# Kernel tuning notes

Measured on AMD Instinct MI355X. Metric: run time of the kernel, lower is better.

Reference implementation:

```python
import jax, jax.numpy as jnp
import numpy as np

N_PATHOLOGY = 14      # NUM_PATHOLOGY_NODES (CheXpert/NIH pathology count)
NEG_SLOPE = 0.2       # PyG GATv2Conv default negative_slope


def gatv2_layer(x, src, dst, n_nodes, Wl, bl, Wr, br, att, bias, concat):
    """PyG GATv2Conv (share_weights=False, dropout inactive in eval).
    Wl/bl: source (lin_l) transform; Wr/br: target (lin_r) transform.
    att: [H, C] attention vector; bias: output bias.
    """
    H, C = att.shape
    xl = (x @ Wl + bl).reshape(-1, H, C)   # [N, H, C] source features
    xr = (x @ Wr + br).reshape(-1, H, C)   # [N, H, C] target features
    xj = xl[src]                            # [E, H, C] gathered source msgs
    xi = xr[dst]                            # [E, H, C] gathered targets
    s = jax.nn.leaky_relu(xi + xj, NEG_SLOPE)
    e = jnp.einsum('ehc,hc->eh', s, att)    # [E, H] raw attention logits
    # segment softmax over incoming edges of each destination node
    m = jax.ops.segment_max(e, dst, num_segments=n_nodes)      # [N, H]
    e = jnp.exp(e - m[dst])
    denom = jax.ops.segment_sum(e, dst, num_segments=n_nodes)  # [N, H]
    alpha = e / (denom[dst] + 1e-16)
    out = jax.ops.segment_sum(alpha[:, :, None] * xj, dst, num_segments=n_nodes)
    out = out.reshape(n_nodes, H * C) if concat else out.mean(axis=1)
    return out + bias


def setup_inputs() -> dict:
    key = jax.random.key(0)
    ks = jax.random.split(key, 16)
    N, E, D, H = 10000, 50000, 768, 4
    s = 0.02
    inp = {
        'x': jax.random.normal(ks[0], (N, D), jnp.float32),
        'edge_index': jax.random.randint(ks[1], (2, E), 0, N, jnp.int32),
        # layer 1: in=768 -> heads=4, out=768 (concat -> 3072)
        'Wl1': jax.random.normal(ks[2], (D, H * D), jnp.float32) * s,
        'bl1': jnp.zeros((H * D,), jnp.float32),
        'Wr1': jax.random.normal(ks[3], (D, H * D), jnp.float32) * s,
        'br1': jnp.zeros((H * D,), jnp.float32),
        'att1': jax.random.normal(ks[4], (H, D), jnp.float32) * s,
        'bias1': jnp.zeros((H * D,), jnp.float32),
        # layer 2: in=3072 -> heads=1, out=768 (mean/no-concat)
        'Wl2': jax.random.normal(ks[5], (H * D, D), jnp.float32) * s,
        'bl2': jnp.zeros((D,), jnp.float32),
        'Wr2': jax.random.normal(ks[6], (H * D, D), jnp.float32) * s,
        'br2': jnp.zeros((D,), jnp.float32),
        'att2': jax.random.normal(ks[7], (1, D), jnp.float32) * s,
        'bias2': jnp.zeros((D,), jnp.float32),
    }
    return inp


def reference(x, edge_index, Wl1, bl1, Wr1, br1, att1, bias1,
              Wl2, bl2, Wr2, br2, att2, bias2):
    n = x.shape[0]
    # PyG GATv2Conv adds self loops by default
    loops = jnp.arange(n, dtype=edge_index.dtype)
    src = jnp.concatenate([edge_index[0], loops])
    dst = jnp.concatenate([edge_index[1], loops])
    h = gatv2_layer(x, src, dst, n, Wl1, bl1, Wr1, br1, att1, bias1, True)
    h = jax.nn.relu(h)  # dropout is identity in eval mode
    out = gatv2_layer(h, src, dst, n, Wl2, bl2, Wr2, br2, att2, bias2, False)
    return out[:N_PATHOLOGY]
```

## Files before the change

kernel.cpp:

```cpp
#include <hip/hip_runtime.h>
#include <cstdint>
#include <cstddef>

#define N_PATH 14
#define NEG_SLOPE 0.2f
#define BINW 128
#define NZ2 4

using u16 = unsigned short;
using u32 = unsigned int;
typedef __attribute__((ext_vector_type(4))) float f32x4;
typedef __attribute__((ext_vector_type(8))) short bf16x8;

__device__ __forceinline__ float lrelu(float v) { return v > 0.f ? v : NEG_SLOPE * v; }
__device__ __forceinline__ u16 f2bf(float f) {
    union { float f; u32 u; } c; c.f = f;
    return (u16)((c.u + 0x7FFFu + ((c.u >> 16) & 1u)) >> 16);
}
__device__ __forceinline__ float bf2f(u16 v) {
    union { u32 u; float f; } c; c.u = ((u32)v) << 16; return c.f;
}
__device__ __forceinline__ int imin(int a, int b) { return a < b ? a : b; }

__global__ void k_init(int* __restrict__ mapBC, int nMap,
                       u32* __restrict__ z, int nZ)
{
    int stride = gridDim.x * blockDim.x;
    int i0 = blockIdx.x * blockDim.x + threadIdx.x;
    for (int i = i0; i < nMap; i += stride) mapBC[i] = -1;
    for (int i = i0; i < nZ; i += stride) z[i] = 0;
}

__global__ void k_build2(const int* __restrict__ esrc, const int* __restrict__ edst,
                         int E, int Nn,
                         int* __restrict__ mapB, int* __restrict__ listB,
                         int* __restrict__ cnt,
                         int* __restrict__ deg2, int* __restrict__ e2bin,
                         int capB)
{
    int e = blockIdx.x * blockDim.x + threadIdx.x;
    int ET = E + Nn;
    if (e >= ET) return;
    int s, d;
    if (e < E) { s = esrc[e]; d = edst[e]; } else { s = e - E; d = s; }
    if (d >= N_PATH) return;
    int slot = atomicAdd(&deg2[d], 1);
    if (slot < BINW) e2bin[d * BINW + slot] = s;
    int old = atomicCAS(&mapB[s], -1, -2);
    if (old == -1) {
        int idx = atomicAdd(&cnt[0], 1);
        if (idx < capB) listB[idx] = s;
        mapB[s] = idx;
    }
}

__global__ void k_build1(const int* __restrict__ esrc, const int* __restrict__ edst,
                         int E, int Nn, const float* __restrict__ x,
                         const int* __restrict__ mapB,
                         int* __restrict__ mapC,
                         int* __restrict__ cnt,
                         int* __restrict__ deg1, int* __restrict__ e1bin,
                         u16* __restrict__ Abf,
                         int capB, int capC)
{
    int e = blockIdx.x * blockDim.x + threadIdx.x;
    int ET = E + Nn;
    int lane = threadIdx.x & 63;

    int s = 0;
    int idx = -1;
    if (e < ET) {
        int d;
        if (e < E) { s = esrc[e]; d = edst[e]; } else { s = e - E; d = s; }
        int b = mapB[d];
        if (b >= 0 && b < capB) {
            int slot = atomicAdd(&deg1[b], 1);
            if (slot < BINW) e1bin[b * BINW + slot] = s;
            int old = atomicCAS(&mapC[s], -1, -2);
            if (old == -1) {
                idx = atomicAdd(&cnt[1], 1);
                mapC[s] = idx;
            }
        }
    }

    bool win = (idx >= 0 && idx < capC);
    unsigned long long mask = __ballot(win);
    while (mask) {
        int l = (int)(__ffsll((long long)mask) - 1);
        mask &= mask - 1;
        int wnode = __shfl(s, l);
        int wslot = __shfl(idx, l);
        const float* xr = x + (size_t)wnode * 768 + lane * 12;
        u16* dst = Abf + (size_t)wslot * 768 + lane * 12;
        float4 v0 = *reinterpret_cast<const float4*>(xr);
        float4 v1 = *reinterpret_cast<const float4*>(xr + 4);
        float4 v2 = *reinterpret_cast<const float4*>(xr + 8);
        uint2 o0, o1, o2;
        o0.x = (u32)f2bf(v0.x) | ((u32)f2bf(v0.y) << 16);
        o0.y = (u32)f2bf(v0.z) | ((u32)f2bf(v0.w) << 16);
        o1.x = (u32)f2bf(v1.x) | ((u32)f2bf(v1.y) << 16);
        o1.y = (u32)f2bf(v1.z) | ((u32)f2bf(v1.w) << 16);
        o2.x = (u32)f2bf(v2.x) | ((u32)f2bf(v2.y) << 16);
        o2.y = (u32)f2bf(v2.z) | ((u32)f2bf(v2.w) << 16);
        *reinterpret_cast<uint2*>(dst)     = o0;
        *reinterpret_cast<uint2*>(dst + 4) = o1;
        *reinterpret_cast<uint2*>(dst + 8) = o2;
    }
}

__device__ __forceinline__
void stage_W(const float* __restrict__ W, int ldw, int wKoff, int n0,
             u16* __restrict__ Ws, int nthreads)
{
    int t = threadIdx.x;
    for (int idx = t; idx < 768 * 8; idx += nthreads) {
        int n4 = (idx & 7) << 2;
        int k  = idx >> 3;
        float4 wv = *reinterpret_cast<const float4*>(
            W + (size_t)(wKoff + k) * ldw + n0 + n4);
        int c = (k >> 3) & 7, kl = k & 7;
        int chbase = (k >> 6) * 2048;
        float wa[4] = {wv.x, wv.y, wv.z, wv.w};
        #pragma unroll
        for (int i = 0; i < 4; ++i) {
            int n = n4 + i;
            Ws[chbase + n * 64 + (kl | ((c ^ (n & 7)) << 3))] = f2bf(wa[i]);
        }
    }
}

__global__ __launch_bounds__(512)
void k_gemm1(const u16* __restrict__ Abf,
             const int* __restrict__ listB, const int* __restrict__ mapC,
             const float* __restrict__ Wl1, const float* __restrict__ Wr1,
             const float* __restrict__ bl1, const float* __restrict__ br1,
             u16* __restrict__ XL1, u16* __restrict__ XR1,
             const int* __restrict__ cnt, int capC, int capB)
{
    __shared__ __align__(16) u16 Ws[12 * 2048];
    int blk = blockIdx.x;
    bool isR = blk >= 96;
    int n0 = (isR ? blk - 96 : blk) * 32;
    const float* W    = isR ? Wr1 : Wl1;
    const float* bias = isR ? br1 : bl1;
    u16* Cout = isR ? XR1 : XL1;
    int nC = imin(cnt[1], capC);
    int M  = isR ? imin(cnt[0], capB) : nC;

    stage_W(W, 3072, 0, n0, Ws, 512);
    __syncthreads();

    int t = threadIdx.x;
    int wave = t >> 6, lane = t & 63;
    int lrow = lane & 15, lhi = lane >> 4;
    int x0 = lrow & 7;
    int preB0 = lrow * 64;
    int preB1 = (16 + lrow) * 64;

    float bv0 = bias[n0 + lrow];
    float bv1 = bias[n0 + 16 + lrow];

    int ntiles = (M + 63) >> 6;
    for (int rt = wave; rt < ntiles; rt += 8) {
        const u16* ap0; const u16* ap1; const u16* ap2; const u16* ap3;
        {
            int ar0 = rt * 64 + lrow;       if (ar0 >= M) ar0 = M - 1;
            int ar1 = ar0 + 16;             if (ar1 >= M) ar1 = M - 1;
            int ar2 = rt * 64 + 32 + lrow;  if (ar2 >= M) ar2 = M - 1;
            int ar3 = ar2 + 16;             if (ar3 >= M) ar3 = M - 1;
            int g0 = ar0, g1 = ar1, g2 = ar2, g3 = ar3;
            if (isR) {
                g0 = mapC[listB[ar0]]; if (g0 < 0) g0 = 0; if (g0 >= nC) g0 = nC - 1;
                g1 = mapC[listB[ar1]]; if (g1 < 0) g1 = 0; if (g1 >= nC) g1 = nC - 1;
                g2 = mapC[listB[ar2]]; if (g2 < 0) g2 = 0; if (g2 >= nC) g2 = nC - 1;
                g3 = mapC[listB[ar3]]; if (g3 < 0) g3 = 0; if (g3 >= nC) g3 = nC - 1;
            }
            ap0 = Abf + (size_t)g0 * 768 + lhi * 8;
            ap1 = Abf + (size_t)g1 * 768 + lhi * 8;
            ap2 = Abf + (size_t)g2 * 768 + lhi * 8;
            ap3 = Abf + (size_t)g3 * 768 + lhi * 8;
        }

        f32x4 acc00 = {0,0,0,0}, acc01 = {0,0,0,0};
        f32x4 acc10 = {0,0,0,0}, acc11 = {0,0,0,0};
        f32x4 acc20 = {0,0,0,0}, acc21 = {0,0,0,0};
        f32x4 acc30 = {0,0,0,0}, acc31 = {0,0,0,0};

        #pragma unroll 4
        for (int kst = 0; kst < 24; ++kst) {
            int ch = kst >> 1;
            int sw = ((((kst & 1) << 2) | lhi) ^ x0) << 3;
            bf16x8 b0 = *reinterpret_cast<const bf16x8*>(&Ws[ch * 2048 + preB0 + sw]);
            bf16x8 b1 = *reinterpret_cast<const bf16x8*>(&Ws[ch * 2048 + preB1 + sw]);
            bf16x8 a0 = *reinterpret_cast<const bf16x8*>(ap0 + kst * 32);
            bf16x8 a1 = *reinterpret_cast<const bf16x8*>(ap1 + kst * 32);
            bf16x8 a2 = *reinterpret_cast<const bf16x8*>(ap2 + kst * 32);
            bf16x8 a3 = *reinterpret_cast<const bf16x8*>(ap3 + kst * 32);
            acc00 = __builtin_amdgcn_mfma_f32_16x16x32_bf16(a0, b0, acc00, 0, 0, 0);
            acc01 = __builtin_amdgcn_mfma_f32_16x16x32_bf16(a0, b1, acc01, 0, 0, 0);
            acc10 = __builtin_amdgcn_mfma_f32_16x16x32_bf16(a1, b0, acc10, 0, 0, 0);
            acc11 = __builtin_amdgcn_mfma_f32_16x16x32_bf16(a1, b1, acc11, 0, 0, 0);
            acc20 = __builtin_amdgcn_mfma_f32_16x16x32_bf16(a2, b0, acc20, 0, 0, 0);
            acc21 = __builtin_amdgcn_mfma_f32_16x16x32_bf16(a2, b1, acc21, 0, 0, 0);
            acc30 = __builtin_amdgcn_mfma_f32_16x16x32_bf16(a3, b0, acc30, 0, 0, 0);
            acc31 = __builtin_amdgcn_mfma_f32_16x16x32_bf16(a3, b1, acc31, 0, 0, 0);
        }

        int gc0 = n0 + lrow, gc1 = n0 + 16 + lrow;
        #pragma unroll
        for (int j = 0; j < 4; ++j) {
            int r0 = rt * 64 + lhi * 4 + j;
            int r1 = r0 + 16, r2 = r0 + 32, r3 = r0 + 48;
            if (r0 < M) {
                Cout[(size_t)r0 * 3072 + gc0] = f2bf(acc00[j] + bv0);
                Cout[(size_t)r0 * 3072 + gc1] = f2bf(acc01[j] + bv1);
            }
            if (r1 < M) {
                Cout[(size_t)r1 * 3072 + gc0] = f2bf(acc10[j] + bv0);
                Cout[(size_t)r1 * 3072 + gc1] = f2bf(acc11[j] + bv1);
            }
            if (r2 < M) {
                Cout[(size_t)r2 * 3072 + gc0] = f2bf(acc20[j] + bv0);
                Cout[(size_t)r2 * 3072 + gc1] = f2bf(acc21[j] + bv1);
            }
            if (r3 < M) {
                Cout[(size_t)r3 * 3072 + gc0] = f2bf(acc30[j] + bv0);
                Cout[(size_t)r3 * 3072 + gc1] = f2bf(acc31[j] + bv1);
            }
        }
    }
}

__global__ __launch_bounds__(256)
void k_gemm2(const u16* __restrict__ H1bf,
             const float* __restrict__ Wl2, const float* __restrict__ Wr2,
             float* __restrict__ XLR2,
             const int* __restrict__ cnt, int capB)
{
    __shared__ __align__(16) u16 Ws[12 * 2048];
    int strip = blockIdx.x;
    int z = blockIdx.z;
    int n0g = strip * 32;
    bool hi = n0g >= 768;
    const float* W = hi ? Wr2 : Wl2;
    int n0w = hi ? n0g - 768 : n0g;
    int nB = imin(cnt[0], capB);
    float* Cp = XLR2 + (size_t)z * capB * 1536;

    stage_W(W, 768, z * 768, n0w, Ws, 256);
    __syncthreads();

    int t = threadIdx.x;
    int wave = t >> 6, lane = t & 63;
    int lrow = lane & 15, lhi = lane >> 4;
    int x0 = lrow & 7;
    int preB0 = lrow * 64, preB1 = (16 + lrow) * 64;

    int ntiles = (nB + 31) >> 5;
    for (int rt = wave; rt < ntiles; rt += 4) {
        int ar0 = rt * 32 + lrow;  if (ar0 >= nB) ar0 = nB - 1;
        int ar1 = ar0 + 16;        if (ar1 >= nB) ar1 = nB - 1;
        const u16* ap0 = H1bf + (size_t)ar0 * 3072 + z * 768 + lhi * 8;
        const u16* ap1 = H1bf + (size_t)ar1 * 3072 + z * 768 + lhi * 8;

        f32x4 acc00 = {0,0,0,0}, acc01 = {0,0,0,0};
        f32x4 acc10 = {0,0,0,0}, acc11 = {0,0,0,0};

        #pragma unroll 4
        for (int kst = 0; kst < 24; ++kst) {
            int ch = kst >> 1;
            int sw = ((((kst & 1) << 2) | lhi) ^ x0) << 3;
            bf16x8 b0 = *reinterpret_cast<const bf16x8*>(&Ws[ch * 2048 + preB0 + sw]);
            bf16x8 b1 = *reinterpret_cast<const bf16x8*>(&Ws[ch * 2048 + preB1 + sw]);
            bf16x8 a0 = *reinterpret_cast<const bf16x8*>(ap0 + kst * 32);
            bf16x8 a1 = *reinterpret_cast<const bf16x8*>(ap1 + kst * 32);
            acc00 = __builtin_amdgcn_mfma_f32_16x16x32_bf16(a0, b0, acc00, 0, 0, 0);
            acc01 = __builtin_amdgcn_mfma_f32_16x16x32_bf16(a0, b1, acc01, 0, 0, 0);
            acc10 = __builtin_amdgcn_mfma_f32_16x16x32_bf16(a1, b0, acc10, 0, 0, 0);
            acc11 = __builtin_amdgcn_mfma_f32_16x16x32_bf16(a1, b1, acc11, 0, 0, 0);
        }

        int gc0 = n0g + lrow, gc1 = n0g + 16 + lrow;
        #pragma unroll
        for (int j = 0; j < 4; ++j) {
            int r0 = rt * 32 + lhi * 4 + j;
            int r1 = r0 + 16;
            if (r0 < nB) {
                Cp[(size_t)r0 * 1536 + gc0] = acc00[j];
                Cp[(size_t)r0 * 1536 + gc1] = acc01[j];
            }
            if (r1 < nB) {
                Cp[(size_t)r1 * 1536 + gc0] = acc10[j];
                Cp[(size_t)r1 * 1536 + gc1] = acc11[j];
            }
        }
    }
}

__global__ __launch_bounds__(256)
void k_fused1(const u16* __restrict__ XL1, const u16* __restrict__ XR1,
              const float* __restrict__ att1, const float* __restrict__ bias1,
              const int* __restrict__ mapC,
              const int* __restrict__ deg1, const int* __restrict__ e1bin,
              u16* __restrict__ H1bf,
              const int* __restrict__ cnt, int capB, int capC)
{
    __shared__ int sIdx[BINW];
    int b = blockIdx.x;
    int nB = cnt[0]; if (nB > capB) nB = capB;
    if (b >= nB) return;
    int t = threadIdx.x;
    int n = deg1[b]; if (n > BINW) n = BINW;
    if (t < n) {
        int c = mapC[e1bin[b * BINW + t]];
        if (c < 0) c = 0; if (c >= capC) c = capC - 1;
        sIdx[t] = c;
    }
    __syncthreads();

    int base = t * 12;
    float xr[12], av[12];
    {
        const u16* p = XR1 + (size_t)b * 3072 + base;
        uint2 q0 = *reinterpret_cast<const uint2*>(p);
        uint2 q1 = *reinterpret_cast<const uint2*>(p + 4);
        uint2 q2 = *reinterpret_cast<const uint2*>(p + 8);
        u32 w[6] = {q0.x, q0.y, q1.x, q1.y, q2.x, q2.y};
        #pragma unroll
        for (int j = 0; j < 6; ++j) {
            xr[2*j]   = bf2f((u16)(w[j] & 0xFFFF));
            xr[2*j+1] = bf2f((u16)(w[j] >> 16));
        }
        float4 a0 = *reinterpret_cast<const float4*>(att1 + base);
        float4 a1 = *reinterpret_cast<const float4*>(att1 + base + 4);
        float4 a2 = *reinterpret_cast<const float4*>(att1 + base + 8);
        av[0]=a0.x; av[1]=a0.y; av[2]=a0.z; av[3]=a0.w;
        av[4]=a1.x; av[5]=a1.y; av[6]=a1.z; av[7]=a1.w;
        av[8]=a2.x; av[9]=a2.y; av[10]=a2.z; av[11]=a2.w;
    }

    float acc[12];
    #pragma unroll
    for (int j = 0; j < 12; ++j) acc[j] = 0.f;
    float sumex = 0.f;

    uint2 q0, q1, q2;
    if (n > 0) {
        const u16* p = XL1 + (size_t)sIdx[0] * 3072 + base;
        q0 = *reinterpret_cast<const uint2*>(p);
        q1 = *reinterpret_cast<const uint2*>(p + 4);
        q2 = *reinterpret_cast<const uint2*>(p + 8);
    }
    for (int i = 0; i < n; ++i) {
        uint2 r0 = q0, r1 = q1, r2 = q2;
        if (i + 1 < n) {
            const u16* p = XL1 + (size_t)sIdx[i + 1] * 3072 + base;
            q0 = *reinterpret_cast<const uint2*>(p);
            q1 = *reinterpret_cast<const uint2*>(p + 4);
            q2 = *reinterpret_cast<const uint2*>(p + 8);
        }
        float xl[12];
        u32 w[6] = {r0.x, r0.y, r1.x, r1.y, r2.x, r2.y};
        #pragma unroll
        for (int j = 0; j < 6; ++j) {
            xl[2*j]   = bf2f((u16)(w[j] & 0xFFFF));
            xl[2*j+1] = bf2f((u16)(w[j] >> 16));
        }
        float pa = 0.f;
        #pragma unroll
        for (int j = 0; j < 12; ++j)
            pa = fmaf(av[j], lrelu(xl[j] + xr[j]), pa);
        #pragma unroll
        for (int off = 32; off > 0; off >>= 1) pa += __shfl_xor(pa, off);
        float ex = expf(pa);
        sumex += ex;
        #pragma unroll
        for (int j = 0; j < 12; ++j) acc[j] = fmaf(ex, xl[j], acc[j]);
    }

    float inv = 1.f / (sumex + 1e-16f);
    u32 o[6];
    #pragma unroll
    for (int j = 0; j < 6; ++j) {
        float v0 = acc[2*j]   * inv + bias1[base + 2*j];
        float v1 = acc[2*j+1] * inv + bias1[base + 2*j+1];
        v0 = v0 > 0.f ? v0 : 0.f;
        v1 = v1 > 0.f ? v1 : 0.f;
        o[j] = (u32)f2bf(v0) | ((u32)f2bf(v1) << 16);
    }
    u16* q = H1bf + (size_t)b * 3072 + base;
    uint2 s0; s0.x = o[0]; s0.y = o[1];
    uint2 s1; s1.x = o[2]; s1.y = o[3];
    uint2 s2; s2.x = o[4]; s2.y = o[5];
    *reinterpret_cast<uint2*>(q)     = s0;
    *reinterpret_cast<uint2*>(q + 4) = s1;
    *reinterpret_cast<uint2*>(q + 8) = s2;
}

__global__ __launch_bounds__(256)
void k_fused2(const float* __restrict__ XLR2,
              const float* __restrict__ att2, const float* __restrict__ bias2,
              const float* __restrict__ bl2, const float* __restrict__ br2,
              const int* __restrict__ mapB,
              const int* __restrict__ deg2, const int* __restrict__ e2bin,
              float* __restrict__ out, int capB)
{
    __shared__ int sIdx[BINW];
    __shared__ float sAcc[4][768];
    __shared__ float sSum[4];
    const size_t PART = (size_t)capB * 1536;
    int a = blockIdx.x;
    int t = threadIdx.x;
    int wv = t >> 6, lane = t & 63;
    int n = deg2[a]; if (n > BINW) n = BINW;
    if (t < n) {
        int bs = mapB[e2bin[a * BINW + t]];
        if (bs < 0) bs = 0; if (bs >= capB) bs = capB - 1;
        sIdx[t] = bs;
    }
    __syncthreads();

    int base = lane * 12;
    int bd = mapB[a];
    if (bd < 0) bd = 0; if (bd >= capB) bd = capB - 1;

    float xr[12], av[12], blv[12];
    {
        const float* p = XLR2 + (size_t)bd * 1536 + 768 + base;
        #pragma unroll
        for (int j = 0; j < 12; ++j) xr[j] = br2[base + j];
        for (int z = 0; z < NZ2; ++z)
            #pragma unroll
            for (int j = 0; j < 12; ++j) xr[j] += p[z * PART + j];
        #pragma unroll
        for (int j = 0; j < 12; ++j) { av[j] = att2[base + j]; blv[j] = bl2[base + j]; }
    }

    float acc[12];
    #pragma unroll
    for (int j = 0; j < 12; ++j) acc[j] = 0.f;
    float sumex = 0.f;

    for (int i = wv; i < n; i += 4) {
        int bs = sIdx[i];
        const float* p = XLR2 + (size_t)bs * 1536 + base;
        float xl[12];
        #pragma unroll
        for (int j = 0; j < 12; ++j) xl[j] = blv[j];
        for (int z = 0; z < NZ2; ++z)
            #pragma unroll
            for (int j = 0; j < 12; ++j) xl[j] += p[z * PART + j];
        float pa = 0.f;
        #pragma unroll
        for (int j = 0; j < 12; ++j)
            pa = fmaf(av[j], lrelu(xl[j] + xr[j]), pa);
        #pragma unroll
        for (int off = 32; off > 0; off >>= 1) pa += __shfl_xor(pa, off);
        float ex = expf(pa);
        sumex += ex;
        #pragma unroll
        for (int j = 0; j < 12; ++j) acc[j] = fmaf(ex, xl[j], acc[j]);
    }

    if (lane == 0) sSum[wv] = sumex;
    #pragma unroll
    for (int j = 0; j < 12; ++j) sAcc[wv][base + j] = acc[j];
    __syncthreads();

    float tot = sSum[0] + sSum[1] + sSum[2] + sSum[3];
    float inv = 1.f / (tot + 1e-16f);
    for (int c = t; c < 768; c += 256) {
        float s = sAcc[0][c] + sAcc[1][c] + sAcc[2][c] + sAcc[3][c];
        out[(size_t)a * 768 + c] = s * inv + bias2[c];
    }
}

struct Lay {
    size_t mapB, mapC;
    size_t zbase, zbytes;
    size_t cnt, deg2, deg1;
    size_t listB, e1bin, e2bin;
    size_t Abf, XL1, XR1, H1bf, XLR2;
    size_t total;
};

static Lay makeLayout(int Nn, int cB, int cC)
{
    Lay L{};
    size_t off = 0;
    auto take = [&](size_t bytes) { size_t o = (off + 255) & ~(size_t)255; off = o + bytes; return o; };
    L.mapB = take((size_t)2 * Nn * 4);
    L.mapC = L.mapB + (size_t)Nn * 4;
    size_t zo = 0;
    size_t cntO  = zo; zo += 64;
    size_t deg2O = zo; zo += 64 * 4;
    size_t deg1O = zo; zo += (size_t)cB * 4;
    L.zbase = take(zo); L.zbytes = zo;
    L.cnt  = L.zbase + cntO;
    L.deg2 = L.zbase + deg2O;
    L.deg1 = L.zbase + deg1O;
    L.listB = take((size_t)cB * 4);
    L.e1bin = take((size_t)cB * BINW * 4);
    L.e2bin = take((size_t)16 * BINW * 4);
    L.Abf  = take((size_t)cC * 768 * 2);
    L.XL1  = take((size_t)cC * 3072 * 2);
    L.XR1  = take((size_t)cB * 3072 * 2);
    L.H1bf = take((size_t)cB * 3072 * 2);
    L.XLR2 = take((size_t)NZ2 * cB * 1536 * 4);
    L.total = off;
    return L;
}

extern "C" void kernel_launch(void* const* d_in, const int* in_sizes, int n_in,
                              void* d_out, int out_size, void* d_ws, size_t ws_size,
                              hipStream_t stream)
{
    const float* x     = (const float*)d_in[0];
    const int*   ei    = (const int*)  d_in[1];
    const float* Wl1   = (const float*)d_in[2];
    const float* bl1   = (const float*)d_in[3];
    const float* Wr1   = (const float*)d_in[4];
    const float* br1   = (const float*)d_in[5];
    const float* att1  = (const float*)d_in[6];
    const float* bias1 = (const float*)d_in[7];
    const float* Wl2   = (const float*)d_in[8];
    const float* bl2   = (const float*)d_in[9];
    const float* Wr2   = (const float*)d_in[10];
    const float* br2   = (const float*)d_in[11];
    const float* att2  = (const float*)d_in[12];
    const float* bias2 = (const float*)d_in[13];
    float* out = (float*)d_out;

    int Nn = in_sizes[0] / 768;
    int E  = in_sizes[1] / 2;
    const int* esrc = ei;
    const int* edst = ei + E;
    int ET = E + Nn;

    static const int tiers[2][2] = { {256, 1024}, {128, 768} };
    int capB = tiers[1][0], capC = tiers[1][1];
    Lay L = makeLayout(Nn, capB, capC);
    for (int t = 0; t < 2; ++t) {
        Lay cand = makeLayout(Nn, tiers[t][0], tiers[t][1]);
        if (cand.total <= ws_size) { capB = tiers[t][0]; capC = tiers[t][1]; L = cand; break; }
    }

    char* ws = (char*)d_ws;
    int*   mapB  = (int*)  (ws + L.mapB);
    int*   mapC  = (int*)  (ws + L.mapC);
    int*   cnt   = (int*)  (ws + L.cnt);
    int*   deg2  = (int*)  (ws + L.deg2);
    int*   deg1  = (int*)  (ws + L.deg1);
    int*   listB = (int*)  (ws + L.listB);
    int*   e1bin = (int*)  (ws + L.e1bin);
    int*   e2bin = (int*)  (ws + L.e2bin);
    u16*   Abf   = (u16*)  (ws + L.Abf);
    u16*   XL1   = (u16*)  (ws + L.XL1);
    u16*   XR1   = (u16*)  (ws + L.XR1);
    u16*   H1bf  = (u16*)  (ws + L.H1bf);
    float* XLR2  = (float*)(ws + L.XLR2);

    k_init<<<256, 256, 0, stream>>>((int*)(ws + L.mapB), 2 * Nn,
                                    (u32*)(ws + L.zbase), (int)(L.zbytes / 4));

    int bgrid = (ET + 255) / 256;
    k_build2<<<bgrid, 256, 0, stream>>>(esrc, edst, E, Nn, mapB, listB, cnt,
                                        deg2, e2bin, capB);
    k_build1<<<bgrid, 256, 0, stream>>>(esrc, edst, E, Nn, x, mapB, mapC, cnt,
                                        deg1, e1bin, Abf, capB, capC);

    k_gemm1<<<192, 512, 0, stream>>>(Abf, listB, mapC, Wl1, Wr1, bl1, br1,
                                     XL1, XR1, cnt, capC, capB);

    k_fused1<<<capB, 256, 0, stream>>>(XL1, XR1, att1, bias1, mapC, deg1, e1bin,
                                       H1bf, cnt, capB, capC);

    k_gemm2<<<dim3(48, 1, NZ2), 256, 0, stream>>>(H1bf, Wl2, Wr2, XLR2, cnt, capB);

    k_fused2<<<N_PATH, 256, 0, stream>>>(XLR2, att2, bias2, bl2, br2, mapB,
                                         deg2, e2bin, out, capB);
}
```

Before: 79.28 us.

## Merge graph-building kernels into one persistent kernel with grid barrier

```diff
diff --git a/kernel.cpp b/kernel.cpp
--- a/kernel.cpp
+++ b/kernel.cpp
@@ -6,6 +6,8 @@
 #define NEG_SLOPE 0.2f
 #define BINW 128
 #define NZ2 4
+#define PBLK 32
+#define PTHR 512
 
 using u16 = unsigned short;
 using u32 = unsigned int;
@@ -22,90 +24,103 @@
 }
 __device__ __forceinline__ int imin(int a, int b) { return a < b ? a : b; }
 
-__global__ void k_init(int* __restrict__ mapBC, int nMap,
-                       u32* __restrict__ z, int nZ)
-{
-    int stride = gridDim.x * blockDim.x;
-    int i0 = blockIdx.x * blockDim.x + threadIdx.x;
-    for (int i = i0; i < nMap; i += stride) mapBC[i] = -1;
-    for (int i = i0; i < nZ; i += stride) z[i] = 0;
-}
-
-__global__ void k_build2(const int* __restrict__ esrc, const int* __restrict__ edst,
-                         int E, int Nn,
-                         int* __restrict__ mapB, int* __restrict__ listB,
-                         int* __restrict__ cnt,
-                         int* __restrict__ deg2, int* __restrict__ e2bin,
-                         int capB)
-{
-    int e = blockIdx.x * blockDim.x + threadIdx.x;
-    int ET = E + Nn;
-    if (e >= ET) return;
-    int s, d;
-    if (e < E) { s = esrc[e]; d = edst[e]; } else { s = e - E; d = s; }
-    if (d >= N_PATH) return;
-    int slot = atomicAdd(&deg2[d], 1);
-    if (slot < BINW) e2bin[d * BINW + slot] = s;
-    int old = atomicCAS(&mapB[s], -1, -2);
-    if (old == -1) {
-        int idx = atomicAdd(&cnt[0], 1);
-        if (idx < capB) listB[idx] = s;
-        mapB[s] = idx;
-    }
-}
-
-__global__ void k_build1(const int* __restrict__ esrc, const int* __restrict__ edst,
-                         int E, int Nn, const float* __restrict__ x,
-                         const int* __restrict__ mapB,
-                         int* __restrict__ mapC,
-                         int* __restrict__ cnt,
-                         int* __restrict__ deg1, int* __restrict__ e1bin,
-                         u16* __restrict__ Abf,
-                         int capB, int capC)
-{
-    int e = blockIdx.x * blockDim.x + threadIdx.x;
+__device__ __forceinline__ void gridbar(unsigned* bar, unsigned& mygen)
+{
+    __syncthreads();
+    if (threadIdx.x == 0) {
+        __threadfence();
+        unsigned nblk = gridDim.x;
+        unsigned prev = atomicAdd(&bar[0], 1u);
+        if (prev == nblk - 1u) {
+            atomicExch(&bar[0], 0u);
+            __threadfence();
+            atomicAdd(&bar[1], 1u);
+        } else {
+            unsigned g;
+            do {
+                __builtin_amdgcn_s_sleep(8);
+                g = __hip_atomic_load(&bar[1], __ATOMIC_RELAXED, __HIP_MEMORY_SCOPE_AGENT);
+            } while (g == mygen);
+        }
+        mygen++;
+        __threadfence();
+    }
+    __syncthreads();
+}
+
+__global__ __launch_bounds__(PTHR)
+void k_prep(const int* __restrict__ esrc, const int* __restrict__ edst,
+            int E, int Nn, const float* __restrict__ x,
+            int* __restrict__ mapB, int* __restrict__ mapC,
+            int* __restrict__ cnt, unsigned* __restrict__ bar,
+            int* __restrict__ deg2, int* __restrict__ deg1,
+            int* __restrict__ listB, int* __restrict__ e2bin,
+            int* __restrict__ e1bin, u16* __restrict__ Abf,
+            int capB, int capC)
+{
+    unsigned mygen = 0;
+    int gtid = blockIdx.x * blockDim.x + threadIdx.x;
+    int gstride = gridDim.x * blockDim.x;
     int ET = E + Nn;
     int lane = threadIdx.x & 63;
 
-    int s = 0;
-    int idx = -1;
-    if (e < ET) {
-        int d;
+    for (int e = gtid; e < ET; e += gstride) {
+        int s, d;
         if (e < E) { s = esrc[e]; d = edst[e]; } else { s = e - E; d = s; }
-        int b = mapB[d];
-        if (b >= 0 && b < capB) {
-            int slot = atomicAdd(&deg1[b], 1);
-            if (slot < BINW) e1bin[b * BINW + slot] = s;
-            int old = atomicCAS(&mapC[s], -1, -2);
-            if (old == -1) {
-                idx = atomicAdd(&cnt[1], 1);
-                mapC[s] = idx;
-            }
-        }
-    }
-
-    bool win = (idx >= 0 && idx < capC);
-    unsigned long long mask = __ballot(win);
-    while (mask) {
-        int l = (int)(__ffsll((long long)mask) - 1);
-        mask &= mask - 1;
-        int wnode = __shfl(s, l);
-        int wslot = __shfl(idx, l);
-        const float* xr = x + (size_t)wnode * 768 + lane * 12;
-        u16* dst = Abf + (size_t)wslot * 768 + lane * 12;
-        float4 v0 = *reinterpret_cast<const float4*>(xr);
-        float4 v1 = *reinterpret_cast<const float4*>(xr + 4);
-        float4 v2 = *reinterpret_cast<const float4*>(xr + 8);
-        uint2 o0, o1, o2;
-        o0.x = (u32)f2bf(v0.x) | ((u32)f2bf(v0.y) << 16);
-        o0.y = (u32)f2bf(v0.z) | ((u32)f2bf(v0.w) << 16);
-        o1.x = (u32)f2bf(v1.x) | ((u32)f2bf(v1.y) << 16);
-        o1.y = (u32)f2bf(v1.z) | ((u32)f2bf(v1.w) << 16);
-        o2.x = (u32)f2bf(v2.x) | ((u32)f2bf(v2.y) << 16);
-        o2.y = (u32)f2bf(v2.z) | ((u32)f2bf(v2.w) << 16);
-        *reinterpret_cast<uint2*>(dst)     = o0;
-        *reinterpret_cast<uint2*>(dst + 4) = o1;
-        *reinterpret_cast<uint2*>(dst + 8) = o2;
+        if (d >= N_PATH) continue;
+        int slot = atomicAdd(&deg2[d], 1);
+        if (slot < BINW) e2bin[d * BINW + slot] = s;
+        int old = atomicCAS(&mapB[s], 0, -2);
+        if (old == 0) {
+            int idx = atomicAdd(&cnt[0], 1);
+            if (idx < capB) listB[idx] = s;
+            mapB[s] = idx + 1;
+        }
+    }
+    gridbar(bar, mygen);
+
+    int niter = (ET + gstride - 1) / gstride;
+    for (int it = 0; it < niter; ++it) {
+        int e = gtid + it * gstride;
+        int s = 0, idx = -1;
+        if (e < ET) {
+            int d;
+            if (e < E) { s = esrc[e]; d = edst[e]; } else { s = e - E; d = s; }
+            int bv = mapB[d];
+            if (bv >= 1 && bv <= capB) {
+                int b = bv - 1;
+                int slot = atomicAdd(&deg1[b], 1);
+                if (slot < BINW) e1bin[b * BINW + slot] = s;
+                int old = atomicCAS(&mapC[s], 0, -2);
+                if (old == 0) {
+                    idx = atomicAdd(&cnt[1], 1);
+                    mapC[s] = idx + 1;
+                }
+            }
+        }
+        bool win = (idx >= 0 && idx < capC);
+        unsigned long long mask = __ballot(win);
+        while (mask) {
+            int l = (int)(__ffsll((long long)mask) - 1);
+            mask &= mask - 1;
+            int wnode = __shfl(s, l);
+            int wslot = __shfl(idx, l);
+            const float* xr = x + (size_t)wnode * 768 + lane * 12;
+            u16* dst = Abf + (size_t)wslot * 768 + lane * 12;
+            float4 v0 = *reinterpret_cast<const float4*>(xr);
+            float4 v1 = *reinterpret_cast<const float4*>(xr + 4);
+            float4 v2 = *reinterpret_cast<const float4*>(xr + 8);
+            uint2 o0, o1, o2;
+            o0.x = (u32)f2bf(v0.x) | ((u32)f2bf(v0.y) << 16);
+            o0.y = (u32)f2bf(v0.z) | ((u32)f2bf(v0.w) << 16);
+            o1.x = (u32)f2bf(v1.x) | ((u32)f2bf(v1.y) << 16);
+            o1.y = (u32)f2bf(v1.z) | ((u32)f2bf(v1.w) << 16);
+            o2.x = (u32)f2bf(v2.x) | ((u32)f2bf(v2.y) << 16);
+            o2.y = (u32)f2bf(v2.z) | ((u32)f2bf(v2.w) << 16);
+            *reinterpret_cast<uint2*>(dst)     = o0;
+            *reinterpret_cast<uint2*>(dst + 4) = o1;
+            *reinterpret_cast<uint2*>(dst + 8) = o2;
+        }
     }
 }
 
@@ -171,10 +186,10 @@
             int ar3 = ar2 + 16;             if (ar3 >= M) ar3 = M - 1;
             int g0 = ar0, g1 = ar1, g2 = ar2, g3 = ar3;
             if (isR) {
-                g0 = mapC[listB[ar0]]; if (g0 < 0) g0 = 0; if (g0 >= nC) g0 = nC - 1;
-                g1 = mapC[listB[ar1]]; if (g1 < 0) g1 = 0; if (g1 >= nC) g1 = nC - 1;
-                g2 = mapC[listB[ar2]]; if (g2 < 0) g2 = 0; if (g2 >= nC) g2 = nC - 1;
-                g3 = mapC[listB[ar3]]; if (g3 < 0) g3 = 0; if (g3 >= nC) g3 = nC - 1;
+                g0 = mapC[listB[ar0]] - 1; if (g0 < 0) g0 = 0; if (g0 >= nC) g0 = nC - 1;
+                g1 = mapC[listB[ar1]] - 1; if (g1 < 0) g1 = 0; if (g1 >= nC) g1 = nC - 1;
+                g2 = mapC[listB[ar2]] - 1; if (g2 < 0) g2 = 0; if (g2 >= nC) g2 = nC - 1;
+                g3 = mapC[listB[ar3]] - 1; if (g3 < 0) g3 = 0; if (g3 >= nC) g3 = nC - 1;
             }
             ap0 = Abf + (size_t)g0 * 768 + lhi * 8;
             ap1 = Abf + (size_t)g1 * 768 + lhi * 8;
@@ -313,7 +328,7 @@
     int t = threadIdx.x;
     int n = deg1[b]; if (n > BINW) n = BINW;
     if (t < n) {
-        int c = mapC[e1bin[b * BINW + t]];
+        int c = mapC[e1bin[b * BINW + t]] - 1;
         if (c < 0) c = 0; if (c >= capC) c = capC - 1;
         sIdx[t] = c;
     }
@@ -415,14 +430,14 @@
     int wv = t >> 6, lane = t & 63;
     int n = deg2[a]; if (n > BINW) n = BINW;
     if (t < n) {
-        int bs = mapB[e2bin[a * BINW + t]];
+        int bs = mapB[e2bin[a * BINW + t]] - 1;
         if (bs < 0) bs = 0; if (bs >= capB) bs = capB - 1;
         sIdx[t] = bs;
     }
     __syncthreads();
 
     int base = lane * 12;
-    int bd = mapB[a];
+    int bd = mapB[a] - 1;
     if (bd < 0) bd = 0; if (bd >= capB) bd = capB - 1;
 
     float xr[12], av[12], blv[12];
@@ -477,9 +492,8 @@
 }
 
 struct Lay {
-    size_t mapB, mapC;
-    size_t zbase, zbytes;
-    size_t cnt, deg2, deg1;
+    size_t zero, zeroBytes;
+    size_t mapB, mapC, cnt, bar, deg2, deg1;
     size_t listB, e1bin, e2bin;
     size_t Abf, XL1, XR1, H1bf, XLR2;
     size_t total;
@@ -490,16 +504,14 @@
     Lay L{};
     size_t off = 0;
     auto take = [&](size_t bytes) { size_t o = (off + 255) & ~(size_t)255; off = o + bytes; return o; };
-    L.mapB = take((size_t)2 * Nn * 4);
+    size_t zb = (size_t)(2 * Nn + 16 + 16 + 64 + cB) * 4;
+    L.zero = take(zb); L.zeroBytes = zb;
+    L.mapB = L.zero;
     L.mapC = L.mapB + (size_t)Nn * 4;
-    size_t zo = 0;
-    size_t cntO  = zo; zo += 64;
-    size_t deg2O = zo; zo += 64 * 4;
-    size_t deg1O = zo; zo += (size_t)cB * 4;
-    L.zbase = take(zo); L.zbytes = zo;
-    L.cnt  = L.zbase + cntO;
-    L.deg2 = L.zbase + deg2O;
-    L.deg1 = L.zbase + deg1O;
+    L.cnt  = L.mapC + (size_t)Nn * 4;
+    L.bar  = L.cnt + 16 * 4;
+    L.deg2 = L.bar + 16 * 4;
+    L.deg1 = L.deg2 + 64 * 4;
     L.listB = take((size_t)cB * 4);
     L.e1bin = take((size_t)cB * BINW * 4);
     L.e2bin = take((size_t)16 * BINW * 4);
@@ -536,7 +548,6 @@
     int E  = in_sizes[1] / 2;
     const int* esrc = ei;
     const int* edst = ei + E;
-    int ET = E + Nn;
 
     static const int tiers[2][2] = { {256, 1024}, {128, 768} };
     int capB = tiers[1][0], capC = tiers[1][1];
@@ -547,28 +558,26 @@
     }
 
     char* ws = (char*)d_ws;
-    int*   mapB  = (int*)  (ws + L.mapB);
-    int*   mapC  = (int*)  (ws + L.mapC);
-    int*   cnt   = (int*)  (ws + L.cnt);
-    int*   deg2  = (int*)  (ws + L.deg2);
-    int*   deg1  = (int*)  (ws + L.deg1);
-    int*   listB = (int*)  (ws + L.listB);
-    int*   e1bin = (int*)  (ws + L.e1bin);
-    int*   e2bin = (int*)  (ws + L.e2bin);
-    u16*   Abf   = (u16*)  (ws + L.Abf);
-    u16*   XL1   = (u16*)  (ws + L.XL1);
-    u16*   XR1   = (u16*)  (ws + L.XR1);
-    u16*   H1bf  = (u16*)  (ws + L.H1bf);
-    float* XLR2  = (float*)(ws + L.XLR2);
-
-    k_init<<<256, 256, 0, stream>>>((int*)(ws + L.mapB), 2 * Nn,
-                                    (u32*)(ws + L.zbase), (int)(L.zbytes / 4));
-
-    int bgrid = (ET + 255) / 256;
-    k_build2<<<bgrid, 256, 0, stream>>>(esrc, edst, E, Nn, mapB, listB, cnt,
-                                        deg2, e2bin, capB);
-    k_build1<<<bgrid, 256, 0, stream>>>(esrc, edst, E, Nn, x, mapB, mapC, cnt,
-                                        deg1, e1bin, Abf, capB, capC);
+    int*      mapB  = (int*)     (ws + L.mapB);
+    int*      mapC  = (int*)     (ws + L.mapC);
+    int*      cnt   = (int*)     (ws + L.cnt);
+    unsigned* bar   = (unsigned*)(ws + L.bar);
+    int*      deg2  = (int*)     (ws + L.deg2);
+    int*      deg1  = (int*)     (ws + L.deg1);
+    int*      listB = (int*)     (ws + L.listB);
+    int*      e1bin = (int*)     (ws + L.e1bin);
+    int*      e2bin = (int*)     (ws + L.e2bin);
+    u16*      Abf   = (u16*)     (ws + L.Abf);
+    u16*      XL1   = (u16*)     (ws + L.XL1);
+    u16*      XR1   = (u16*)     (ws + L.XR1);
+    u16*      H1bf  = (u16*)     (ws + L.H1bf);
+    float*    XLR2  = (float*)   (ws + L.XLR2);
+
+    hipMemsetAsync(ws + L.zero, 0, L.zeroBytes, stream);
+
+    k_prep<<<PBLK, PTHR, 0, stream>>>(esrc, edst, E, Nn, x,
+                                      mapB, mapC, cnt, bar, deg2, deg1,
+                                      listB, e2bin, e1bin, Abf, capB, capC);
 
     k_gemm1<<<192, 512, 0, stream>>>(Abf, listB, mapC, Wl1, Wr1, bl1, br1,
                                      XL1, XR1, cnt, capC, capB);
```

Result: slower. 85.34 us (+7.6%).
